# Optimization experiments

Measured on AMD Instinct MI355X. Metric: run time of the kernel, lower is better.

The kernel has to match this reference:

```python
import jax, jax.numpy as jnp
import numpy as np
from jax import lax

B, S, F, H, A, C = 256, 128, 128, 512, 512, 128


def _gru_cell(x, h, Wih, Whh, bih, bhh):
    # PyTorch GRU cell: gates ordered (r, z, n)
    gi = x @ Wih.T + bih            # [B, 3H]
    gh = h @ Whh.T + bhh            # [B, 3H]
    ir, iz, inn = jnp.split(gi, 3, axis=-1)
    hr, hz, hn = jnp.split(gh, 3, axis=-1)
    r = jax.nn.sigmoid(ir + hr)
    z = jax.nn.sigmoid(iz + hz)
    n = jnp.tanh(inn + r * hn)
    return (1.0 - z) * n + z * h


def setup_inputs() -> dict:
    key = jax.random.key(0)
    ks = jax.random.split(key, 13)
    def n(k, shape, s=0.05):
        return jax.random.normal(k, shape, dtype=jnp.float32) * s
    return dict(
        x=n(ks[0], (B, S, F), 1.0),
        y=jax.random.randint(ks[1], (B, C), 0, S),
        enc_Wih=n(ks[2], (3 * H, F)), enc_Whh=n(ks[3], (3 * H, H)),
        enc_bih=n(ks[4], (3 * H,)), enc_bhh=n(ks[5], (3 * H,)),
        dec_Wih=n(ks[6], (3 * H, F)), dec_Whh=n(ks[7], (3 * H, H)),
        dec_bih=n(ks[8], (3 * H,)), dec_bhh=n(ks[9], (3 * H,)),
        w1=n(ks[10], (A, H)), w2=n(ks[11], (A, H)), v=n(ks[12], (A,)),
    )


def reference(x, y, enc_Wih, enc_Whh, enc_bih, enc_bhh,
              dec_Wih, dec_Whh, dec_bih, dec_bhh, w1, w2, v):
    b, s, f = x.shape
    c = y.shape[1]
    h0 = jnp.zeros((b, H), x.dtype)

    # ---- encoder GRU over sequence ----
    def enc_step(h, xt):
        h2 = _gru_cell(xt, h, enc_Wih, enc_Whh, enc_bih, enc_bhh)
        return h2, h2
    hT, enc_out = lax.scan(enc_step, h0, jnp.swapaxes(x, 0, 1))  # enc_out [S,B,H]
    enc_out = jnp.swapaxes(enc_out, 0, 1)                        # [B,S,H]

    # w1(enc_out) is loop-invariant: precompute (same math as recomputing per step)
    enc_proj = jnp.einsum('bsh,ah->bsa', enc_out, w1)            # [B,S,A]

    # ---- decoder pointer loop (teacher_force_ratio=0.0 -> always use argmax) ----
    def dec_step(carry, y_i):
        h, dec_in = carry
        h = _gru_cell(dec_in, h, dec_Wih, dec_Whh, dec_bih, dec_bhh)  # [B,H]
        att = jax.nn.relu(enc_proj + (h @ w2.T)[:, None, :])          # [B,S,A]
        prob = jax.nn.softmax(jnp.einsum('bsa,a->bs', att, v), axis=1)  # [B,S]
        # faithful to original: F.cross_entropy applied to probabilities
        logp = jax.nn.log_softmax(prob, axis=1)
        step_loss = -jnp.mean(jnp.take_along_axis(logp, y_i[:, None], axis=1))
        pred = jnp.argmax(prob, axis=1)                               # [B]
        dec_in_next = jnp.take_along_axis(x, pred[:, None, None], axis=1)[:, 0, :]
        return (h, dec_in_next), (pred, step_loss)

    dec_in0 = jnp.zeros((b, f), x.dtype)
    (_, _), (preds, losses) = lax.scan(dec_step, (hT, dec_in0), y.T)
    preds = preds.T                                   # [B, C]
    loss = jnp.sum(losses) / b / c
    return preds, loss
```

## Files before the change

kernel.cpp:

```cpp
#include <hip/hip_runtime.h>
#include <math.h>

#define B_ 256
#define S_ 128
#define F_ 128
#define H_ 512
#define A_ 512
#define C_ 128

#define DOT4(va, vb) ((va).x*(vb).x + (va).y*(vb).y + (va).z*(vb).z + (va).w*(vb).w)

__global__ __launch_bounds__(256)
void transpose_x(const float* __restrict__ x, float* __restrict__ xT)
{
    const int t = blockIdx.x >> 2;
    const int f0 = (blockIdx.x & 3) * 32;
    const int b = threadIdx.x;
#pragma unroll 4
    for (int ff = 0; ff < 32; ++ff) {
        int f = f0 + ff;
        xT[(size_t)t * (F_ * B_) + (size_t)f * B_ + b] =
            x[(size_t)b * (S_ * F_) + (size_t)t * F_ + f];
    }
}

__global__ __launch_bounds__(256)
void prep_w6(const float* __restrict__ Wih, const float* __restrict__ Whh,
             float* __restrict__ W6)
{
    int id = blockIdx.x * 256 + threadIdx.x;
    if (id >= 256 * 640 * 6) return;
    int up = id / 3840;
    int rem = id - up * 3840;
    int k = rem / 6, g = rem - k * 6;
    int row = (g >> 1) * H_ + up * 2 + (g & 1);
    float val;
    if (k < F_) val = Wih[(size_t)row * F_ + k];
    else        val = Whh[(size_t)row * H_ + (k - F_)];
    W6[id] = val;
}

__global__ __launch_bounds__(256)
void prep_w2q(const float* __restrict__ w2, float4* __restrict__ w2q,
              float* __restrict__ dec_inT)
{
    int id = blockIdx.x * 256 + threadIdx.x;
    if (id < 128 * 512) {
        int k4 = id >> 9, a = id & 511;
        const float* s = w2 + (size_t)a * H_ + k4 * 4;
        w2q[id] = make_float4(s[0], s[1], s[2], s[3]);
    }
    if (id < F_ * B_) dec_inT[id] = 0.f;
}

__global__ __launch_bounds__(256)
void prep_bias(const float* __restrict__ ebih, const float* __restrict__ ebhh,
               const float* __restrict__ dbih, const float* __restrict__ dbhh,
               float* __restrict__ bias4e, float* __restrict__ bias4d,
               float* __restrict__ h0T, int* __restrict__ eflags,
               int* __restrict__ dflags)
{
    int id = blockIdx.x * 256 + threadIdx.x;
    if (id < H_ * B_) h0T[id] = 0.f;
    if (id < 256 * 32) { eflags[id] = 0; dflags[id] = 0; }
    if (id < H_) {
        bias4e[id * 4 + 0] = ebih[id] + ebhh[id];
        bias4e[id * 4 + 1] = ebih[H_ + id] + ebhh[H_ + id];
        bias4e[id * 4 + 2] = ebih[2 * H_ + id];
        bias4e[id * 4 + 3] = ebhh[2 * H_ + id];
        bias4d[id * 4 + 0] = dbih[id] + dbhh[id];
        bias4d[id * 4 + 1] = dbih[H_ + id] + dbhh[H_ + id];
        bias4d[id * 4 + 2] = dbih[2 * H_ + id];
        bias4d[id * 4 + 3] = dbhh[2 * H_ + id];
    }
}

template<int NH>
__device__ __forceinline__ void acc_range(const float* __restrict__ src,
                                          const float* __restrict__ W6k,
                                          int nk, int b, float* __restrict__ acc)
{
    float a0[8], a1[8];
#pragma unroll
    for (int j = 0; j < 8; ++j) a0[j] = src[(size_t)j * B_ + b];
    for (int kc = 0; kc < nk; kc += 8) {
        if (kc + 8 < nk) {
#pragma unroll
            for (int j = 0; j < 8; ++j) a1[j] = src[(size_t)(kc + 8 + j) * B_ + b];
        }
        const float* Wr = W6k + (size_t)kc * 6;
#pragma unroll
        for (int j = 0; j < 8; ++j) {
            float av = a0[j];
            acc[0]      = fmaf(av, Wr[j * 6 + 0], acc[0]);
            acc[1]      = fmaf(av, Wr[j * 6 + 1], acc[1]);
            acc[2]      = fmaf(av, Wr[j * 6 + 2], acc[2]);
            acc[3]      = fmaf(av, Wr[j * 6 + 3], acc[3]);
            acc[NH]     = fmaf(av, Wr[j * 6 + 4], acc[NH]);
            acc[NH + 1] = fmaf(av, Wr[j * 6 + 5], acc[NH + 1]);
        }
#pragma unroll
        for (int j = 0; j < 8; ++j) a0[j] = a1[j];
    }
}

__device__ __forceinline__ void wait_all_blocks(const int* __restrict__ flags,
                                                int tid, int target)
{
    if (tid < 64) {
        while (true) {
            int mn = 0x7fffffff;
#pragma unroll
            for (int q = 0; q < 4; ++q) {
                int vq = __hip_atomic_load(&flags[(tid + q * 64) * 32],
                                           __ATOMIC_RELAXED,
                                           __HIP_MEMORY_SCOPE_AGENT);
                mn = vq < mn ? vq : mn;
            }
            if (__all(mn >= target)) break;
            __builtin_amdgcn_s_sleep(2);
        }
    }
}

__global__ __launch_bounds__(512)
void enc_persist(const float* __restrict__ xT,
                 const float* __restrict__ W6,
                 const float* __restrict__ bias4,
                 const float* __restrict__ h0T,
                 float* __restrict__ encT,
                 int* __restrict__ eflags)
{
    __shared__ float accL[256][6];
    const int tid = threadIdx.x;
    const int lane = tid & 63;
    const int w = tid >> 6;
    const int bg = w & 3;
    const int kw = w >> 2;
    const int b = bg * 64 + lane;
    const int up = blockIdx.x;
    const float* Wb = W6 + (size_t)up * (640 * 6);
    const int u0 = up * 2, u1 = u0 + 1;
    const float4 bb0 = *(const float4*)(bias4 + u0 * 4);
    const float4 bb1 = *(const float4*)(bias4 + u1 * 4);

    for (int t = 0; t < S_; ++t) {
        const float* inT = xT + (size_t)t * (F_ * B_);
        const float* hinT = (t == 0) ? h0T : encT + (size_t)(t - 1) * (H_ * B_);
        float* houtT = encT + (size_t)t * (H_ * B_);

        float acc[8];
#pragma unroll
        for (int g = 0; g < 8; ++g) acc[g] = 0.f;

        if (kw == 0) acc_range<4>(inT, Wb, F_, b, acc);

        if (t > 0) wait_all_blocks(eflags, tid, t);
        __syncthreads();

        if (kw == 0) {
            acc_range<6>(hinT, Wb + F_ * 6, 192, b, acc);
        } else {
            acc_range<6>(hinT + (size_t)192 * B_, Wb + 320 * 6, 320, b, acc);
        }

        if (kw == 1) {
            const int li = tid & 255;
            accL[li][0] = acc[0]; accL[li][1] = acc[1];
            accL[li][2] = acc[2]; accL[li][3] = acc[3];
            accL[li][4] = acc[6]; accL[li][5] = acc[7];
        }
        __syncthreads();
        if (kw == 0) {
            float rr0 = 1.f / (1.f + expf(-(acc[0] + accL[tid][0] + bb0.x)));
            float rr1 = 1.f / (1.f + expf(-(acc[1] + accL[tid][1] + bb1.x)));
            float zz0 = 1.f / (1.f + expf(-(acc[2] + accL[tid][2] + bb0.y)));
            float zz1 = 1.f / (1.f + expf(-(acc[3] + accL[tid][3] + bb1.y)));
            float hn0 = acc[6] + accL[tid][4] + bb0.w;
            float hn1 = acc[7] + accL[tid][5] + bb1.w;
            float nn0 = tanhf(acc[4] + bb0.z + rr0 * hn0);
            float nn1 = tanhf(acc[5] + bb1.z + rr1 * hn1);
            float ho0 = hinT[(size_t)u0 * B_ + b];
            float ho1 = hinT[(size_t)u1 * B_ + b];
            float h0v = (1.f - zz0) * nn0 + zz0 * ho0;
            float h1v = (1.f - zz1) * nn1 + zz1 * ho1;
            __hip_atomic_store(&houtT[(size_t)u0 * B_ + b], h0v,
                               __ATOMIC_RELAXED, __HIP_MEMORY_SCOPE_AGENT);
            __hip_atomic_store(&houtT[(size_t)u1 * B_ + b], h1v,
                               __ATOMIC_RELAXED, __HIP_MEMORY_SCOPE_AGENT);
        }
        asm volatile("s_waitcnt vmcnt(0)" ::: "memory");
        __syncthreads();
        if (tid == 0) {
            __hip_atomic_store(&eflags[up * 32], t + 1,
                               __ATOMIC_RELAXED, __HIP_MEMORY_SCOPE_AGENT);
        }
    }
}

__global__ __launch_bounds__(512)
void dec_fused(const float* __restrict__ dec_in,
               const float* __restrict__ hinT,
               const float* __restrict__ W6,
               const float* __restrict__ bias4,
               float* __restrict__ houtT,
               float* __restrict__ hB,
               const float4* __restrict__ w2q,
               const float* __restrict__ v, const int* __restrict__ y,
               int step, const float* __restrict__ x,
               const float* __restrict__ proj,
               float* __restrict__ dec_out,
               float* __restrict__ nlogp, float* __restrict__ preds_out,
               int* __restrict__ dflags)
{
    __shared__ float accL[256][6];
    __shared__ float sh[512];
    __shared__ float sq[512];
    __shared__ float sScore[S_], sProb[S_];
    __shared__ int sPred;

    const int tid = threadIdx.x;
    const int lane = tid & 63;
    const int w = tid >> 6;
    const int bg = w & 3;
    const int kw = w >> 2;
    const int b = bg * 64 + lane;
    const int up = blockIdx.x;

    {
        const float* Wb = W6 + (size_t)up * (640 * 6);
        float acc[8];
#pragma unroll
        for (int g = 0; g < 8; ++g) acc[g] = 0.f;

        if (kw == 0) {
            acc_range<4>(dec_in, Wb, F_, b, acc);
            acc_range<6>(hinT, Wb + F_ * 6, 192, b, acc);
        } else {
            acc_range<6>(hinT + (size_t)192 * B_, Wb + 320 * 6, 320, b, acc);
        }

        if (kw == 1) {
            const int li = tid & 255;
            accL[li][0] = acc[0]; accL[li][1] = acc[1];
            accL[li][2] = acc[2]; accL[li][3] = acc[3];
            accL[li][4] = acc[6]; accL[li][5] = acc[7];
        }
        __syncthreads();
        if (kw == 0) {
            const int u0 = up * 2, u1 = u0 + 1;
            float4 bb0 = *(const float4*)(bias4 + u0 * 4);
            float4 bb1 = *(const float4*)(bias4 + u1 * 4);
            float rr0 = 1.f / (1.f + expf(-(acc[0] + accL[tid][0] + bb0.x)));
            float rr1 = 1.f / (1.f + expf(-(acc[1] + accL[tid][1] + bb1.x)));
            float zz0 = 1.f / (1.f + expf(-(acc[2] + accL[tid][2] + bb0.y)));
            float zz1 = 1.f / (1.f + expf(-(acc[3] + accL[tid][3] + bb1.y)));
            float hn0 = acc[6] + accL[tid][4] + bb0.w;
            float hn1 = acc[7] + accL[tid][5] + bb1.w;
            float nn0 = tanhf(acc[4] + bb0.z + rr0 * hn0);
            float nn1 = tanhf(acc[5] + bb1.z + rr1 * hn1);
            float ho0 = hinT[(size_t)u0 * B_ + b];
            float ho1 = hinT[(size_t)u1 * B_ + b];
            float h0v = (1.f - zz0) * nn0 + zz0 * ho0;
            float h1v = (1.f - zz1) * nn1 + zz1 * ho1;
            houtT[(size_t)u0 * B_ + b] = h0v;
            houtT[(size_t)u1 * B_ + b] = h1v;
            __hip_atomic_store(&hB[(size_t)b * H_ + u0], h0v,
                               __ATOMIC_RELAXED, __HIP_MEMORY_SCOPE_AGENT);
            __hip_atomic_store(&hB[(size_t)b * H_ + u1], h1v,
                               __ATOMIC_RELAXED, __HIP_MEMORY_SCOPE_AGENT);
        }
        asm volatile("s_waitcnt vmcnt(0)" ::: "memory");
        __syncthreads();
        if (tid == 0) {
            __hip_atomic_store(&dflags[up * 32], step + 1,
                               __ATOMIC_RELAXED, __HIP_MEMORY_SCOPE_AGENT);
        }
    }

    wait_all_blocks(dflags, tid, step + 1);
    __syncthreads();

    const int bb = blockIdx.x;
    sh[tid] = __hip_atomic_load(&hB[(size_t)bb * H_ + tid],
                                __ATOMIC_RELAXED, __HIP_MEMORY_SCOPE_AGENT);
    __syncthreads();

    {
        float acc = 0.f;
        const float4* wp = w2q + tid;
#pragma unroll 8
        for (int k4 = 0; k4 < 128; ++k4) {
            float4 hv = *(const float4*)&sh[k4 * 4];
            float4 wv4 = wp[(size_t)k4 * 512];
            acc += DOT4(hv, wv4);
        }
        sq[tid] = acc;
    }
    __syncthreads();

    const int wv = tid >> 6, ln = tid & 63;
    float4 q0 = *(const float4*)&sq[ln * 8];
    float4 q1 = *(const float4*)&sq[ln * 8 + 4];
    float4 v0r = *(const float4*)(v + ln * 8);
    float4 v1r = *(const float4*)(v + ln * 8 + 4);
    const float* epb = proj + (size_t)bb * (S_ * A_);
    for (int si = 0; si < 16; ++si) {
        int s = si * 8 + wv;
        const float* row = epb + (size_t)s * A_ + ln * 8;
        float4 p0 = *(const float4*)(row);
        float4 p1 = *(const float4*)(row + 4);
        float acc = fmaxf(p0.x + q0.x, 0.f) * v0r.x
                  + fmaxf(p0.y + q0.y, 0.f) * v0r.y
                  + fmaxf(p0.z + q0.z, 0.f) * v0r.z
                  + fmaxf(p0.w + q0.w, 0.f) * v0r.w
                  + fmaxf(p1.x + q1.x, 0.f) * v1r.x
                  + fmaxf(p1.y + q1.y, 0.f) * v1r.y
                  + fmaxf(p1.z + q1.z, 0.f) * v1r.z
                  + fmaxf(p1.w + q1.w, 0.f) * v1r.w;
#pragma unroll
        for (int off = 32; off; off >>= 1) acc += __shfl_down(acc, off);
        if (ln == 0) sScore[s] = acc;
    }
    __syncthreads();

    if (tid < 64) {
        float s0v = sScore[tid], s1v = sScore[tid + 64];
        float m = fmaxf(s0v, s1v);
#pragma unroll
        for (int off = 32; off; off >>= 1) m = fmaxf(m, __shfl_xor(m, off));
        float e0 = expf(s0v - m), e1 = expf(s1v - m);
        float se = e0 + e1;
#pragma unroll
        for (int off = 32; off; off >>= 1) se += __shfl_xor(se, off);
        float p0 = e0 / se, p1 = e1 / se;
        sProb[tid] = p0; sProb[tid + 64] = p1;
        float pm = fmaxf(p0, p1);
#pragma unroll
        for (int off = 32; off; off >>= 1) pm = fmaxf(pm, __shfl_xor(pm, off));
        float t0 = expf(p0 - pm), t1 = expf(p1 - pm);
        float T = t0 + t1;
#pragma unroll
        for (int off = 32; off; off >>= 1) T += __shfl_xor(T, off);
        float bv = p0; int bi2 = tid;
        if (p1 > bv) { bv = p1; bi2 = tid + 64; }
#pragma unroll
        for (int off = 32; off; off >>= 1) {
            float ov = __shfl_xor(bv, off);
            int oi = __shfl_xor(bi2, off);
            if (ov > bv || (ov == bv && oi < bi2)) { bv = ov; bi2 = oi; }
        }
        if (tid == 0) {
            sPred = bi2;
            int yy = y[(size_t)bb * C_ + step];
            float py = sProb[yy];
            nlogp[(size_t)step * B_ + bb] = -(py - pm - logf(T));
            preds_out[(size_t)bb * C_ + step] = (float)bi2;
        }
    }
    __syncthreads();

    const int pred = sPred;
    if (tid < F_) {
        dec_out[(size_t)tid * B_ + bb] = x[((size_t)bb * S_ + pred) * F_ + tid];
    }
}

__global__ __launch_bounds__(256)
void proj_gemm(const float* __restrict__ encT, const float* __restrict__ w1,
               float* __restrict__ proj)
{
    __shared__ float sA[32][128];
    __shared__ float sB[32][128];
    const int tid = threadIdx.x;
    const int s = blockIdx.z;
    const int b0 = blockIdx.y * 128;
    const int a0 = blockIdx.x * 128;
    const int tx = tid & 15, ty = tid >> 4;

    float acc[8][8];
#pragma unroll
    for (int i = 0; i < 8; ++i)
#pragma unroll
        for (int j = 0; j < 8; ++j) acc[i][j] = 0.f;

    const float* Abase = encT + (size_t)s * (H_ * B_) + b0;
    for (int kc = 0; kc < H_; kc += 32) {
#pragma unroll
        for (int p = 0; p < 16; ++p) {
            int idx = tid + p * 256;
            int kj = idx >> 7, bbb = idx & 127;
            sA[kj][bbb] = Abase[(size_t)(kc + kj) * B_ + bbb];
        }
#pragma unroll
        for (int p = 0; p < 16; ++p) {
            int idx = tid + p * 256;
            int aa = idx >> 5, kj = idx & 31;
            sB[kj][aa] = w1[(size_t)(a0 + aa) * H_ + kc + kj];
        }
        __syncthreads();
#pragma unroll
        for (int kj = 0; kj < 32; ++kj) {
            float4 af0 = *(const float4*)&sA[kj][ty * 8];
            float4 af1 = *(const float4*)&sA[kj][ty * 8 + 4];
            float4 bf0 = *(const float4*)&sB[kj][tx * 8];
            float4 bf1 = *(const float4*)&sB[kj][tx * 8 + 4];
            float am[8] = {af0.x, af0.y, af0.z, af0.w, af1.x, af1.y, af1.z, af1.w};
            float bn[8] = {bf0.x, bf0.y, bf0.z, bf0.w, bf1.x, bf1.y, bf1.z, bf1.w};
#pragma unroll
            for (int i = 0; i < 8; ++i)
#pragma unroll
                for (int j = 0; j < 8; ++j)
                    acc[i][j] = fmaf(am[i], bn[j], acc[i][j]);
        }
        __syncthreads();
    }
#pragma unroll
    for (int i = 0; i < 8; ++i) {
        float* dst = proj + ((size_t)(b0 + ty * 8 + i) * S_ + s) * A_ + a0 + tx * 8;
        *(float4*)(dst) = make_float4(acc[i][0], acc[i][1], acc[i][2], acc[i][3]);
        *(float4*)(dst + 4) = make_float4(acc[i][4], acc[i][5], acc[i][6], acc[i][7]);
    }
}

__global__ void final_loss(const float* __restrict__ nlogp, float* __restrict__ out)
{
    __shared__ float part[C_];
    const int i = threadIdx.x;
    float s = 0.f;
    for (int b = 0; b < B_; ++b) s += nlogp[(size_t)i * B_ + b];
    part[i] = s / (float)B_;
    __syncthreads();
    if (i == 0) {
        float t = 0.f;
        for (int k = 0; k < C_; ++k) t += part[k];
        out[0] = t / (float)B_ / (float)C_;
    }
}

extern "C" void kernel_launch(void* const* d_in, const int* in_sizes, int n_in,
                              void* d_out, int out_size, void* d_ws, size_t ws_size,
                              hipStream_t stream)
{
    (void)in_sizes; (void)n_in; (void)out_size; (void)ws_size;
    const float* x    = (const float*)d_in[0];
    const int*   y    = (const int*)d_in[1];
    const float* eWih = (const float*)d_in[2];
    const float* eWhh = (const float*)d_in[3];
    const float* ebih = (const float*)d_in[4];
    const float* ebhh = (const float*)d_in[5];
    const float* dWih = (const float*)d_in[6];
    const float* dWhh = (const float*)d_in[7];
    const float* dbih = (const float*)d_in[8];
    const float* dbhh = (const float*)d_in[9];
    const float* w1   = (const float*)d_in[10];
    const float* w2   = (const float*)d_in[11];
    const float* v    = (const float*)d_in[12];
    float* out = (float*)d_out;

    float* ws = (float*)d_ws;
    float* encT    = ws;
    float* W6d     = ws;
    float* w2qf    = ws + 983040;
    float* hT0     = ws + 1245184;
    float* hT1     = ws + 1376256;
    float* dec_inT = ws + 1507328;
    float* nlogp   = ws + 1540096;
    float* hB      = ws + 1572864;
    float* encT127 = ws + 16646144;
    float* projB   = ws + 16777216;
    float* xT      = projB;
    float* W6e     = projB + 4194304;
    float* h0T     = projB + 5177344;
    float* bias4e  = ws + 33554432;
    float* bias4d  = bias4e + 2048;
    int*   eflags  = (int*)(bias4d + 2048);
    int*   dflags  = eflags + 256 * 32;

    prep_bias<<<dim3(512), 256, 0, stream>>>(ebih, ebhh, dbih, dbhh,
                                             bias4e, bias4d, h0T, eflags, dflags);
    transpose_x<<<dim3(512), 256, 0, stream>>>(x, xT);
    prep_w6<<<dim3(3840), 256, 0, stream>>>(eWih, eWhh, W6e);

    {
        void* a[] = { (void*)&xT, (void*)&W6e, (void*)&bias4e, (void*)&h0T,
                      (void*)&encT, (void*)&eflags };
        hipLaunchCooperativeKernel((const void*)enc_persist,
                                   dim3(256), dim3(512), a, 0, stream);
    }

    proj_gemm<<<dim3(4, 2, 128), 256, 0, stream>>>(encT, w1, projB);

    prep_w6<<<dim3(3840), 256, 0, stream>>>(dWih, dWhh, W6d);
    prep_w2q<<<dim3(256), 256, 0, stream>>>(w2, (float4*)w2qf, dec_inT);

    float* hb[2] = { hT0, hT1 };
    for (int i = 0; i < C_; ++i) {
        const float* hin = (i == 0) ? encT127 : hb[(i & 1) ^ 1];
        float* hout = hb[i & 1];
        dec_fused<<<dim3(256), 512, 0, stream>>>(
            dec_inT, hin, W6d, bias4d, hout, hB, (const float4*)w2qf, v, y,
            i, x, projB, dec_inT, nlogp, out, dflags);
    }

    final_loss<<<dim3(1), 128, 0, stream>>>(nlogp, out + (size_t)B_ * C_);
}
```

Before: 8.785 ms.

## Make decoder a persistent cooperative kernel with flag-based grid sync and retiled GRU

```diff
diff --git a/kernel.cpp b/kernel.cpp
--- a/kernel.cpp
+++ b/kernel.cpp
@@ -8,7 +8,55 @@
 #define A_ 512
 #define C_ 128
 
-#define DOT4(va, vb) ((va).x*(vb).x + (va).y*(vb).y + (va).z*(vb).z + (va).w*(vb).w)
+template<bool SC1>
+__device__ __forceinline__ float ldf(const float* p)
+{
+    if constexpr (SC1)
+        return __hip_atomic_load(p, __ATOMIC_RELAXED, __HIP_MEMORY_SCOPE_AGENT);
+    else
+        return *p;
+}
+
+__device__ __forceinline__ void stf(float* p, float v)
+{
+    __hip_atomic_store(p, v, __ATOMIC_RELAXED, __HIP_MEMORY_SCOPE_AGENT);
+}
+
+__device__ __forceinline__ void spin_flag(const int* f, int target)
+{
+    while (__hip_atomic_load(f, __ATOMIC_RELAXED, __HIP_MEMORY_SCOPE_AGENT) < target)
+        __builtin_amdgcn_s_sleep(1);
+}
+
+template<int NH, bool SC1>
+__device__ __forceinline__ void acc_chunks(const float* __restrict__ src,
+                                           const float* __restrict__ W6k,
+                                           int nk, int b, float* __restrict__ acc)
+{
+    float a0[32], a1[32];
+#pragma unroll
+    for (int j = 0; j < 32; ++j) a0[j] = ldf<SC1>(src + (size_t)j * B_ + b);
+    for (int kc = 0; kc < nk; kc += 32) {
+        if (kc + 32 < nk) {
+#pragma unroll
+            for (int j = 0; j < 32; ++j)
+                a1[j] = ldf<SC1>(src + (size_t)(kc + 32 + j) * B_ + b);
+        }
+        const float* Wr = W6k + (size_t)kc * 6;
+#pragma unroll
+        for (int j = 0; j < 32; ++j) {
+            float av = a0[j];
+            acc[0]    = fmaf(av, Wr[j * 6 + 0], acc[0]);
+            acc[1]    = fmaf(av, Wr[j * 6 + 1], acc[1]);
+            acc[2]    = fmaf(av, Wr[j * 6 + 2], acc[2]);
+            acc[3]    = fmaf(av, Wr[j * 6 + 3], acc[3]);
+            acc[NH]   = fmaf(av, Wr[j * 6 + 4], acc[NH]);
+            acc[NH+1] = fmaf(av, Wr[j * 6 + 5], acc[NH + 1]);
+        }
+#pragma unroll
+        for (int j = 0; j < 32; ++j) a0[j] = a1[j];
+    }
+}
 
 __global__ __launch_bounds__(256)
 void transpose_x(const float* __restrict__ x, float* __restrict__ xT)
@@ -26,9 +74,10 @@
 
 __global__ __launch_bounds__(256)
 void prep_w6(const float* __restrict__ Wih, const float* __restrict__ Whh,
-             float* __restrict__ W6)
+             float* __restrict__ W6, float* __restrict__ zbuf, int zn)
 {
     int id = blockIdx.x * 256 + threadIdx.x;
+    if (zbuf && id < zn) zbuf[id] = 0.f;
     if (id >= 256 * 640 * 6) return;
     int up = id / 3840;
     int rem = id - up * 3840;
@@ -38,19 +87,6 @@
     if (k < F_) val = Wih[(size_t)row * F_ + k];
     else        val = Whh[(size_t)row * H_ + (k - F_)];
     W6[id] = val;
-}
-
-__global__ __launch_bounds__(256)
-void prep_w2q(const float* __restrict__ w2, float4* __restrict__ w2q,
-              float* __restrict__ dec_inT)
-{
-    int id = blockIdx.x * 256 + threadIdx.x;
-    if (id < 128 * 512) {
-        int k4 = id >> 9, a = id & 511;
-        const float* s = w2 + (size_t)a * H_ + k4 * 4;
-        w2q[id] = make_float4(s[0], s[1], s[2], s[3]);
-    }
-    if (id < F_ * B_) dec_inT[id] = 0.f;
 }
 
 __global__ __launch_bounds__(256)
@@ -75,54 +111,6 @@
     }
 }
 
-template<int NH>
-__device__ __forceinline__ void acc_range(const float* __restrict__ src,
-                                          const float* __restrict__ W6k,
-                                          int nk, int b, float* __restrict__ acc)
-{
-    float a0[8], a1[8];
-#pragma unroll
-    for (int j = 0; j < 8; ++j) a0[j] = src[(size_t)j * B_ + b];
-    for (int kc = 0; kc < nk; kc += 8) {
-        if (kc + 8 < nk) {
-#pragma unroll
-            for (int j = 0; j < 8; ++j) a1[j] = src[(size_t)(kc + 8 + j) * B_ + b];
-        }
-        const float* Wr = W6k + (size_t)kc * 6;
-#pragma unroll
-        for (int j = 0; j < 8; ++j) {
-            float av = a0[j];
-            acc[0]      = fmaf(av, Wr[j * 6 + 0], acc[0]);
-            acc[1]      = fmaf(av, Wr[j * 6 + 1], acc[1]);
-            acc[2]      = fmaf(av, Wr[j * 6 + 2], acc[2]);
-            acc[3]      = fmaf(av, Wr[j * 6 + 3], acc[3]);
-            acc[NH]     = fmaf(av, Wr[j * 6 + 4], acc[NH]);
-            acc[NH + 1] = fmaf(av, Wr[j * 6 + 5], acc[NH + 1]);
-        }
-#pragma unroll
-        for (int j = 0; j < 8; ++j) a0[j] = a1[j];
-    }
-}
-
-__device__ __forceinline__ void wait_all_blocks(const int* __restrict__ flags,
-                                                int tid, int target)
-{
-    if (tid < 64) {
-        while (true) {
-            int mn = 0x7fffffff;
-#pragma unroll
-            for (int q = 0; q < 4; ++q) {
-                int vq = __hip_atomic_load(&flags[(tid + q * 64) * 32],
-                                           __ATOMIC_RELAXED,
-                                           __HIP_MEMORY_SCOPE_AGENT);
-                mn = vq < mn ? vq : mn;
-            }
-            if (__all(mn >= target)) break;
-            __builtin_amdgcn_s_sleep(2);
-        }
-    }
-}
-
 __global__ __launch_bounds__(512)
 void enc_persist(const float* __restrict__ xT,
                  const float* __restrict__ W6,
@@ -131,90 +119,88 @@
                  float* __restrict__ encT,
                  int* __restrict__ eflags)
 {
-    __shared__ float accL[256][6];
+    __shared__ float accL[4][64][6];
     const int tid = threadIdx.x;
     const int lane = tid & 63;
     const int w = tid >> 6;
-    const int bg = w & 3;
     const int kw = w >> 2;
-    const int b = bg * 64 + lane;
-    const int up = blockIdx.x;
-    const float* Wb = W6 + (size_t)up * (640 * 6);
+    const int uq = w & 3;
+    const int jb = blockIdx.x >> 2;
+    const int bt = blockIdx.x & 3;
+    const int b = bt * 64 + lane;
+    const int up = jb * 4 + uq;
+    const float* Wb = W6 + (size_t)up * 3840;
     const int u0 = up * 2, u1 = u0 + 1;
     const float4 bb0 = *(const float4*)(bias4 + u0 * 4);
     const float4 bb1 = *(const float4*)(bias4 + u1 * 4);
 
     for (int t = 0; t < S_; ++t) {
         const float* inT = xT + (size_t)t * (F_ * B_);
-        const float* hinT = (t == 0) ? h0T : encT + (size_t)(t - 1) * (H_ * B_);
-        float* houtT = encT + (size_t)t * (H_ * B_);
+        const float* hin = (t == 0) ? h0T : encT + (size_t)(t - 1) * (H_ * B_);
+        float* hout = encT + (size_t)t * (H_ * B_);
 
         float acc[8];
 #pragma unroll
         for (int g = 0; g < 8; ++g) acc[g] = 0.f;
 
-        if (kw == 0) acc_range<4>(inT, Wb, F_, b, acc);
-
-        if (t > 0) wait_all_blocks(eflags, tid, t);
-        __syncthreads();
-
+        if (kw == 0) acc_chunks<4, false>(inT, Wb, F_, b, acc);
+
+        if (t > 0 && tid < 256) spin_flag(&eflags[tid * 32], t);
+        __syncthreads();
+
+        float hold0 = 0.f, hold1 = 0.f;
         if (kw == 0) {
-            acc_range<6>(hinT, Wb + F_ * 6, 192, b, acc);
+            hold0 = hin[(size_t)u0 * B_ + b];
+            hold1 = hin[(size_t)u1 * B_ + b];
+            acc_chunks<6, false>(hin, Wb + F_ * 6, 192, b, acc);
         } else {
-            acc_range<6>(hinT + (size_t)192 * B_, Wb + 320 * 6, 320, b, acc);
+            acc_chunks<6, false>(hin + (size_t)192 * B_, Wb + 320 * 6, 320, b, acc);
         }
 
         if (kw == 1) {
-            const int li = tid & 255;
-            accL[li][0] = acc[0]; accL[li][1] = acc[1];
-            accL[li][2] = acc[2]; accL[li][3] = acc[3];
-            accL[li][4] = acc[6]; accL[li][5] = acc[7];
+            accL[uq][lane][0] = acc[0]; accL[uq][lane][1] = acc[1];
+            accL[uq][lane][2] = acc[2]; accL[uq][lane][3] = acc[3];
+            accL[uq][lane][4] = acc[6]; accL[uq][lane][5] = acc[7];
         }
         __syncthreads();
         if (kw == 0) {
-            float rr0 = 1.f / (1.f + expf(-(acc[0] + accL[tid][0] + bb0.x)));
-            float rr1 = 1.f / (1.f + expf(-(acc[1] + accL[tid][1] + bb1.x)));
-            float zz0 = 1.f / (1.f + expf(-(acc[2] + accL[tid][2] + bb0.y)));
-            float zz1 = 1.f / (1.f + expf(-(acc[3] + accL[tid][3] + bb1.y)));
-            float hn0 = acc[6] + accL[tid][4] + bb0.w;
-            float hn1 = acc[7] + accL[tid][5] + bb1.w;
+            float rr0 = 1.f / (1.f + expf(-(acc[0] + accL[uq][lane][0] + bb0.x)));
+            float rr1 = 1.f / (1.f + expf(-(acc[1] + accL[uq][lane][1] + bb1.x)));
+            float zz0 = 1.f / (1.f + expf(-(acc[2] + accL[uq][lane][2] + bb0.y)));
+            float zz1 = 1.f / (1.f + expf(-(acc[3] + accL[uq][lane][3] + bb1.y)));
+            float hn0 = acc[6] + accL[uq][lane][4] + bb0.w;
+            float hn1 = acc[7] + accL[uq][lane][5] + bb1.w;
             float nn0 = tanhf(acc[4] + bb0.z + rr0 * hn0);
             float nn1 = tanhf(acc[5] + bb1.z + rr1 * hn1);
-            float ho0 = hinT[(size_t)u0 * B_ + b];
-            float ho1 = hinT[(size_t)u1 * B_ + b];
-            float h0v = (1.f - zz0) * nn0 + zz0 * ho0;
-            float h1v = (1.f - zz1) * nn1 + zz1 * ho1;
-            __hip_atomic_store(&houtT[(size_t)u0 * B_ + b], h0v,
+            stf(&hout[(size_t)u0 * B_ + b], (1.f - zz0) * nn0 + zz0 * hold0);
+            stf(&hout[(size_t)u1 * B_ + b], (1.f - zz1) * nn1 + zz1 * hold1);
+        }
+        asm volatile("s_waitcnt vmcnt(0)" ::: "memory");
+        __syncthreads();
+        if (tid == 0) {
+            __hip_atomic_store(&eflags[blockIdx.x * 32], t + 1,
                                __ATOMIC_RELAXED, __HIP_MEMORY_SCOPE_AGENT);
-            __hip_atomic_store(&houtT[(size_t)u1 * B_ + b], h1v,
-                               __ATOMIC_RELAXED, __HIP_MEMORY_SCOPE_AGENT);
-        }
-        asm volatile("s_waitcnt vmcnt(0)" ::: "memory");
-        __syncthreads();
-        if (tid == 0) {
-            __hip_atomic_store(&eflags[up * 32], t + 1,
-                               __ATOMIC_RELAXED, __HIP_MEMORY_SCOPE_AGENT);
         }
     }
 }
 
 __global__ __launch_bounds__(512)
-void dec_fused(const float* __restrict__ dec_in,
-               const float* __restrict__ hinT,
-               const float* __restrict__ W6,
-               const float* __restrict__ bias4,
-               float* __restrict__ houtT,
-               float* __restrict__ hB,
-               const float4* __restrict__ w2q,
-               const float* __restrict__ v, const int* __restrict__ y,
-               int step, const float* __restrict__ x,
-               const float* __restrict__ proj,
-               float* __restrict__ dec_out,
-               float* __restrict__ nlogp, float* __restrict__ preds_out,
-               int* __restrict__ dflags)
-{
-    __shared__ float accL[256][6];
-    __shared__ float sh[512];
+void dec_persist(const float* __restrict__ x,
+                 const int*   __restrict__ y,
+                 const float* __restrict__ W6,
+                 const float* __restrict__ bias4,
+                 const float* __restrict__ w2,
+                 const float* __restrict__ v,
+                 const float* __restrict__ proj,
+                 const float* __restrict__ h_init,
+                 float* __restrict__ hT0, float* __restrict__ hT1,
+                 float* __restrict__ dec_inT,
+                 float* __restrict__ hw2,
+                 float* __restrict__ nlogp, float* __restrict__ preds,
+                 int* __restrict__ dflags)
+{
+    __shared__ float accL[4][64][6];
+    __shared__ float accP[256][8];
     __shared__ float sq[512];
     __shared__ float sScore[S_], sProb[S_];
     __shared__ int sPred;
@@ -222,147 +208,194 @@
     const int tid = threadIdx.x;
     const int lane = tid & 63;
     const int w = tid >> 6;
-    const int bg = w & 3;
     const int kw = w >> 2;
-    const int b = bg * 64 + lane;
-    const int up = blockIdx.x;
-
-    {
-        const float* Wb = W6 + (size_t)up * (640 * 6);
-        float acc[8];
-#pragma unroll
-        for (int g = 0; g < 8; ++g) acc[g] = 0.f;
-
-        if (kw == 0) {
-            acc_range<4>(dec_in, Wb, F_, b, acc);
-            acc_range<6>(hinT, Wb + F_ * 6, 192, b, acc);
-        } else {
-            acc_range<6>(hinT + (size_t)192 * B_, Wb + 320 * 6, 320, b, acc);
-        }
-
-        if (kw == 1) {
-            const int li = tid & 255;
-            accL[li][0] = acc[0]; accL[li][1] = acc[1];
-            accL[li][2] = acc[2]; accL[li][3] = acc[3];
-            accL[li][4] = acc[6]; accL[li][5] = acc[7];
-        }
-        __syncthreads();
-        if (kw == 0) {
-            const int u0 = up * 2, u1 = u0 + 1;
-            float4 bb0 = *(const float4*)(bias4 + u0 * 4);
-            float4 bb1 = *(const float4*)(bias4 + u1 * 4);
-            float rr0 = 1.f / (1.f + expf(-(acc[0] + accL[tid][0] + bb0.x)));
-            float rr1 = 1.f / (1.f + expf(-(acc[1] + accL[tid][1] + bb1.x)));
-            float zz0 = 1.f / (1.f + expf(-(acc[2] + accL[tid][2] + bb0.y)));
-            float zz1 = 1.f / (1.f + expf(-(acc[3] + accL[tid][3] + bb1.y)));
-            float hn0 = acc[6] + accL[tid][4] + bb0.w;
-            float hn1 = acc[7] + accL[tid][5] + bb1.w;
-            float nn0 = tanhf(acc[4] + bb0.z + rr0 * hn0);
-            float nn1 = tanhf(acc[5] + bb1.z + rr1 * hn1);
-            float ho0 = hinT[(size_t)u0 * B_ + b];
-            float ho1 = hinT[(size_t)u1 * B_ + b];
-            float h0v = (1.f - zz0) * nn0 + zz0 * ho0;
-            float h1v = (1.f - zz1) * nn1 + zz1 * ho1;
-            houtT[(size_t)u0 * B_ + b] = h0v;
-            houtT[(size_t)u1 * B_ + b] = h1v;
-            __hip_atomic_store(&hB[(size_t)b * H_ + u0], h0v,
+    const int uq = w & 3;
+    const int jb = blockIdx.x >> 2;
+    const int bt = blockIdx.x & 3;
+    const int b = bt * 64 + lane;
+    const int up = jb * 4 + uq;
+    const float* Wb = W6 + (size_t)up * 3840;
+    const int u0 = up * 2, u1 = u0 + 1;
+    const float4 bb0 = *(const float4*)(bias4 + u0 * 4);
+    const float4 bb1 = *(const float4*)(bias4 + u1 * 4);
+    const float4 v0r = *(const float4*)(v + lane * 8);
+    const float4 v1r = *(const float4*)(v + lane * 8 + 4);
+    const int bid = blockIdx.x;
+
+    for (int st = 0; st < C_; ++st) {
+        const float* hin = (st == 0) ? h_init : ((st & 1) ? hT0 : hT1);
+        float* hout = (st & 1) ? hT1 : hT0;
+
+        {
+            float acc[8];
+#pragma unroll
+            for (int g = 0; g < 8; ++g) acc[g] = 0.f;
+
+            float hold0 = 0.f, hold1 = 0.f;
+            if (kw == 0) {
+                hold0 = ldf<true>(hin + (size_t)u0 * B_ + b);
+                hold1 = ldf<true>(hin + (size_t)u1 * B_ + b);
+                acc_chunks<6, true>(hin, Wb + F_ * 6, 192, b, acc);
+            } else {
+                acc_chunks<6, true>(hin + (size_t)192 * B_, Wb + 320 * 6, 320, b, acc);
+            }
+
+            if (st > 0 && tid < 256) spin_flag(&dflags[tid * 32], 3 * st);
+            __syncthreads();
+
+            if (kw == 0) acc_chunks<4, true>(dec_inT, Wb, F_, b, acc);
+
+            if (kw == 1) {
+                accL[uq][lane][0] = acc[0]; accL[uq][lane][1] = acc[1];
+                accL[uq][lane][2] = acc[2]; accL[uq][lane][3] = acc[3];
+                accL[uq][lane][4] = acc[6]; accL[uq][lane][5] = acc[7];
+            }
+            __syncthreads();
+            if (kw == 0) {
+                float rr0 = 1.f / (1.f + expf(-(acc[0] + accL[uq][lane][0] + bb0.x)));
+                float rr1 = 1.f / (1.f + expf(-(acc[1] + accL[uq][lane][1] + bb1.x)));
+                float zz0 = 1.f / (1.f + expf(-(acc[2] + accL[uq][lane][2] + bb0.y)));
+                float zz1 = 1.f / (1.f + expf(-(acc[3] + accL[uq][lane][3] + bb1.y)));
+                float hn0 = acc[6] + accL[uq][lane][4] + bb0.w;
+                float hn1 = acc[7] + accL[uq][lane][5] + bb1.w;
+                float nn0 = tanhf(acc[4] + bb0.z + rr0 * hn0);
+                float nn1 = tanhf(acc[5] + bb1.z + rr1 * hn1);
+                stf(&hout[(size_t)u0 * B_ + b], (1.f - zz0) * nn0 + zz0 * hold0);
+                stf(&hout[(size_t)u1 * B_ + b], (1.f - zz1) * nn1 + zz1 * hold1);
+            }
+            asm volatile("s_waitcnt vmcnt(0)" ::: "memory");
+            __syncthreads();
+            if (tid == 0)
+                __hip_atomic_store(&dflags[bid * 32], 3 * st + 1,
+                                   __ATOMIC_RELAXED, __HIP_MEMORY_SCOPE_AGENT);
+        }
+
+        if (tid < 256) spin_flag(&dflags[tid * 32], 3 * st + 1);
+        __syncthreads();
+        if (bid < 64) {
+            const int a0 = bid * 8;
+            const int pb = tid & 255;
+            const int kh = tid >> 8;
+            const float* hsrc = hout + (size_t)(kh * 256) * B_;
+            const float* w2b = w2 + (size_t)a0 * H_ + kh * 256;
+            float pacc[8];
+#pragma unroll
+            for (int j = 0; j < 8; ++j) pacc[j] = 0.f;
+            {
+                float c0[32], c1[32];
+#pragma unroll
+                for (int j = 0; j < 32; ++j)
+                    c0[j] = ldf<true>(hsrc + (size_t)j * B_ + pb);
+                for (int kc = 0; kc < 256; kc += 32) {
+                    if (kc + 32 < 256) {
+#pragma unroll
+                        for (int j = 0; j < 32; ++j)
+                            c1[j] = ldf<true>(hsrc + (size_t)(kc + 32 + j) * B_ + pb);
+                    }
+#pragma unroll
+                    for (int j = 0; j < 32; ++j) {
+                        float av = c0[j];
+#pragma unroll
+                        for (int jj = 0; jj < 8; ++jj)
+                            pacc[jj] = fmaf(av, w2b[(size_t)jj * H_ + kc + j], pacc[jj]);
+                    }
+#pragma unroll
+                    for (int j = 0; j < 32; ++j) c0[j] = c1[j];
+                }
+            }
+            if (kh == 1) {
+#pragma unroll
+                for (int j = 0; j < 8; ++j) accP[pb][j] = pacc[j];
+            }
+            __syncthreads();
+            if (kh == 0) {
+#pragma unroll
+                for (int j = 0; j < 8; ++j)
+                    stf(&hw2[(size_t)pb * A_ + a0 + j], pacc[j] + accP[pb][j]);
+            }
+        }
+        asm volatile("s_waitcnt vmcnt(0)" ::: "memory");
+        __syncthreads();
+        if (tid == 0)
+            __hip_atomic_store(&dflags[bid * 32], 3 * st + 2,
                                __ATOMIC_RELAXED, __HIP_MEMORY_SCOPE_AGENT);
-            __hip_atomic_store(&hB[(size_t)b * H_ + u1], h1v,
+
+        if (tid < 256) spin_flag(&dflags[tid * 32], 3 * st + 2);
+        __syncthreads();
+        {
+            const int bb = bid;
+            sq[tid] = ldf<true>(&hw2[(size_t)bb * A_ + tid]);
+            __syncthreads();
+
+            float4 q0 = *(const float4*)&sq[lane * 8];
+            float4 q1 = *(const float4*)&sq[lane * 8 + 4];
+            const float* epb = proj + (size_t)bb * (S_ * A_);
+            for (int si = 0; si < 16; ++si) {
+                int ss = si * 8 + w;
+                const float* row = epb + (size_t)ss * A_ + lane * 8;
+                float4 p0 = *(const float4*)(row);
+                float4 p1 = *(const float4*)(row + 4);
+                float acc = fmaxf(p0.x + q0.x, 0.f) * v0r.x
+                          + fmaxf(p0.y + q0.y, 0.f) * v0r.y
+                          + fmaxf(p0.z + q0.z, 0.f) * v0r.z
+                          + fmaxf(p0.w + q0.w, 0.f) * v0r.w
+                          + fmaxf(p1.x + q1.x, 0.f) * v1r.x
+                          + fmaxf(p1.y + q1.y, 0.f) * v1r.y
+                          + fmaxf(p1.z + q1.z, 0.f) * v1r.z
+                          + fmaxf(p1.w + q1.w, 0.f) * v1r.w;
+#pragma unroll
+                for (int off = 32; off; off >>= 1) acc += __shfl_down(acc, off);
+                if (lane == 0) sScore[ss] = acc;
+            }
+            __syncthreads();
+
+            if (tid < 64) {
+                float s0v = sScore[tid], s1v = sScore[tid + 64];
+                float m = fmaxf(s0v, s1v);
+#pragma unroll
+                for (int off = 32; off; off >>= 1) m = fmaxf(m, __shfl_xor(m, off));
+                float e0 = expf(s0v - m), e1 = expf(s1v - m);
+                float se = e0 + e1;
+#pragma unroll
+                for (int off = 32; off; off >>= 1) se += __shfl_xor(se, off);
+                float p0 = e0 / se, p1 = e1 / se;
+                sProb[tid] = p0; sProb[tid + 64] = p1;
+                float pm = fmaxf(p0, p1);
+#pragma unroll
+                for (int off = 32; off; off >>= 1) pm = fmaxf(pm, __shfl_xor(pm, off));
+                float t0 = expf(p0 - pm), t1 = expf(p1 - pm);
+                float T = t0 + t1;
+#pragma unroll
+                for (int off = 32; off; off >>= 1) T += __shfl_xor(T, off);
+                float bv = p0; int bi2 = tid;
+                if (p1 > bv) { bv = p1; bi2 = tid + 64; }
+#pragma unroll
+                for (int off = 32; off; off >>= 1) {
+                    float ov = __shfl_xor(bv, off);
+                    int oi = __shfl_xor(bi2, off);
+                    if (ov > bv || (ov == bv && oi < bi2)) { bv = ov; bi2 = oi; }
+                }
+                if (tid == 0) {
+                    sPred = bi2;
+                    int yy = y[(size_t)bb * C_ + st];
+                    float py = sProb[yy];
+                    nlogp[(size_t)st * B_ + bb] = -(py - pm - logf(T));
+                    preds[(size_t)bb * C_ + st] = (float)bi2;
+                }
+            }
+            __syncthreads();
+
+            const int pred = sPred;
+            if (tid < F_) {
+                stf(&dec_inT[(size_t)tid * B_ + bb],
+                    x[((size_t)bb * S_ + pred) * F_ + tid]);
+            }
+        }
+        asm volatile("s_waitcnt vmcnt(0)" ::: "memory");
+        __syncthreads();
+        if (tid == 0)
+            __hip_atomic_store(&dflags[bid * 32], 3 * st + 3,
                                __ATOMIC_RELAXED, __HIP_MEMORY_SCOPE_AGENT);
-        }
-        asm volatile("s_waitcnt vmcnt(0)" ::: "memory");
-        __syncthreads();
-        if (tid == 0) {
-            __hip_atomic_store(&dflags[up * 32], step + 1,
-                               __ATOMIC_RELAXED, __HIP_MEMORY_SCOPE_AGENT);
-        }
-    }
-
-    wait_all_blocks(dflags, tid, step + 1);
-    __syncthreads();
-
-    const int bb = blockIdx.x;
-    sh[tid] = __hip_atomic_load(&hB[(size_t)bb * H_ + tid],
-                                __ATOMIC_RELAXED, __HIP_MEMORY_SCOPE_AGENT);
-    __syncthreads();
-
-    {
-        float acc = 0.f;
-        const float4* wp = w2q + tid;
-#pragma unroll 8
-        for (int k4 = 0; k4 < 128; ++k4) {
-            float4 hv = *(const float4*)&sh[k4 * 4];
-            float4 wv4 = wp[(size_t)k4 * 512];
-            acc += DOT4(hv, wv4);
-        }
-        sq[tid] = acc;
-    }
-    __syncthreads();
-
-    const int wv = tid >> 6, ln = tid & 63;
-    float4 q0 = *(const float4*)&sq[ln * 8];
-    float4 q1 = *(const float4*)&sq[ln * 8 + 4];
-    float4 v0r = *(const float4*)(v + ln * 8);
-    float4 v1r = *(const float4*)(v + ln * 8 + 4);
-    const float* epb = proj + (size_t)bb * (S_ * A_);
-    for (int si = 0; si < 16; ++si) {
-        int s = si * 8 + wv;
-        const float* row = epb + (size_t)s * A_ + ln * 8;
-        float4 p0 = *(const float4*)(row);
-        float4 p1 = *(const float4*)(row + 4);
-        float acc = fmaxf(p0.x + q0.x, 0.f) * v0r.x
-                  + fmaxf(p0.y + q0.y, 0.f) * v0r.y
-                  + fmaxf(p0.z + q0.z, 0.f) * v0r.z
-                  + fmaxf(p0.w + q0.w, 0.f) * v0r.w
-                  + fmaxf(p1.x + q1.x, 0.f) * v1r.x
-                  + fmaxf(p1.y + q1.y, 0.f) * v1r.y
-                  + fmaxf(p1.z + q1.z, 0.f) * v1r.z
-                  + fmaxf(p1.w + q1.w, 0.f) * v1r.w;
-#pragma unroll
-        for (int off = 32; off; off >>= 1) acc += __shfl_down(acc, off);
-        if (ln == 0) sScore[s] = acc;
-    }
-    __syncthreads();
-
-    if (tid < 64) {
-        float s0v = sScore[tid], s1v = sScore[tid + 64];
-        float m = fmaxf(s0v, s1v);
-#pragma unroll
-        for (int off = 32; off; off >>= 1) m = fmaxf(m, __shfl_xor(m, off));
-        float e0 = expf(s0v - m), e1 = expf(s1v - m);
-        float se = e0 + e1;
-#pragma unroll
-        for (int off = 32; off; off >>= 1) se += __shfl_xor(se, off);
-        float p0 = e0 / se, p1 = e1 / se;
-        sProb[tid] = p0; sProb[tid + 64] = p1;
-        float pm = fmaxf(p0, p1);
-#pragma unroll
-        for (int off = 32; off; off >>= 1) pm = fmaxf(pm, __shfl_xor(pm, off));
-        float t0 = expf(p0 - pm), t1 = expf(p1 - pm);
-        float T = t0 + t1;
-#pragma unroll
-        for (int off = 32; off; off >>= 1) T += __shfl_xor(T, off);
-        float bv = p0; int bi2 = tid;
-        if (p1 > bv) { bv = p1; bi2 = tid + 64; }
-#pragma unroll
-        for (int off = 32; off; off >>= 1) {
-            float ov = __shfl_xor(bv, off);
-            int oi = __shfl_xor(bi2, off);
-            if (ov > bv || (ov == bv && oi < bi2)) { bv = ov; bi2 = oi; }
-        }
-        if (tid == 0) {
-            sPred = bi2;
-            int yy = y[(size_t)bb * C_ + step];
-            float py = sProb[yy];
-            nlogp[(size_t)step * B_ + bb] = -(py - pm - logf(T));
-            preds_out[(size_t)bb * C_ + step] = (float)bi2;
-        }
-    }
-    __syncthreads();
-
-    const int pred = sPred;
-    if (tid < F_) {
-        dec_out[(size_t)tid * B_ + bb] = x[((size_t)bb * S_ + pred) * F_ + tid];
     }
 }
 
@@ -461,12 +494,11 @@
     float* ws = (float*)d_ws;
     float* encT    = ws;
     float* W6d     = ws;
-    float* w2qf    = ws + 983040;
-    float* hT0     = ws + 1245184;
-    float* hT1     = ws + 1376256;
-    float* dec_inT = ws + 1507328;
-    float* nlogp   = ws + 1540096;
-    float* hB      = ws + 1572864;
+    float* hT0     = ws + 983040;
+    float* hT1     = ws + 1114112;
+    float* dec_inT = ws + 1245184;
+    float* nlogp   = ws + 1277952;
+    float* hw2     = ws + 1310720;
     float* encT127 = ws + 16646144;
     float* projB   = ws + 16777216;
     float* xT      = projB;
@@ -480,7 +512,7 @@
     prep_bias<<<dim3(512), 256, 0, stream>>>(ebih, ebhh, dbih, dbhh,
                                              bias4e, bias4d, h0T, eflags, dflags);
     transpose_x<<<dim3(512), 256, 0, stream>>>(x, xT);
-    prep_w6<<<dim3(3840), 256, 0, stream>>>(eWih, eWhh, W6e);
+    prep_w6<<<dim3(3840), 256, 0, stream>>>(eWih, eWhh, W6e, (float*)nullptr, 0);
 
     {
         void* a[] = { (void*)&xT, (void*)&W6e, (void*)&bias4e, (void*)&h0T,
@@ -491,16 +523,15 @@
 
     proj_gemm<<<dim3(4, 2, 128), 256, 0, stream>>>(encT, w1, projB);
 
-    prep_w6<<<dim3(3840), 256, 0, stream>>>(dWih, dWhh, W6d);
-    prep_w2q<<<dim3(256), 256, 0, stream>>>(w2, (float4*)w2qf, dec_inT);
-
-    float* hb[2] = { hT0, hT1 };
-    for (int i = 0; i < C_; ++i) {
-        const float* hin = (i == 0) ? encT127 : hb[(i & 1) ^ 1];
-        float* hout = hb[i & 1];
-        dec_fused<<<dim3(256), 512, 0, stream>>>(
-            dec_inT, hin, W6d, bias4d, hout, hB, (const float4*)w2qf, v, y,
-            i, x, projB, dec_inT, nlogp, out, dflags);
+    prep_w6<<<dim3(3840), 256, 0, stream>>>(dWih, dWhh, W6d, dec_inT, F_ * B_);
+
+    {
+        void* a[] = { (void*)&x, (void*)&y, (void*)&W6d, (void*)&bias4d,
+                      (void*)&w2, (void*)&v, (void*)&projB, (void*)&encT127,
+                      (void*)&hT0, (void*)&hT1, (void*)&dec_inT, (void*)&hw2,
+                      (void*)&nlogp, (void*)&out, (void*)&dflags };
+        hipLaunchCooperativeKernel((const void*)dec_persist,
+                                   dim3(256), dim3(512), a, 0, stream);
     }
 
     final_loss<<<dim3(1), 128, 0, stream>>>(nlogp, out + (size_t)B_ * C_);
```

Measured after the change: 19.52 ms. 122% more time.
